# Optimization experiments

Hardware: AMD Instinct MI355X
Metric: run time of the kernel (lower is better)

## Reference

```python
import jax, jax.numpy as jnp
import numpy as np

WS = 14          # window size (SAM ViT default)
NUM_HEADS = 12   # dim=768 -> head_dim=64
THETA = 10000.0  # rope theta


def _axial_rope_cos_sin(head_dim, end_x, end_y):
    # compute_axial_cis: head_dim//4 freqs per axis; t_x = t % end_x, t_y = t // end_x
    n = head_dim // 4
    freqs = 1.0 / (THETA ** (np.arange(0, head_dim, 4)[:n].astype(np.float32) / head_dim))
    t = np.arange(end_x * end_y, dtype=np.float32)
    t_x = t % end_x
    t_y = np.floor(t / end_x)
    ang = np.concatenate([t_x[:, None] * freqs[None, :], t_y[:, None] * freqs[None, :]], axis=-1)
    return jnp.asarray(np.cos(ang)), jnp.asarray(np.sin(ang))  # (N, head_dim//2) each


def _apply_rope(x, cos, sin):
    # x: (B, N, D) viewed as complex pairs along last dim (torch.view_as_complex ordering)
    x2 = x.reshape(x.shape[:-1] + (-1, 2))
    xr, xi = x2[..., 0], x2[..., 1]
    out_r = xr * cos - xi * sin
    out_i = xr * sin + xi * cos
    return jnp.stack([out_r, out_i], axis=-1).reshape(x.shape)


def setup_inputs() -> dict:
    key = jax.random.key(0)
    ks = jax.random.split(key, 6)
    B, H, W, C = 8, 64, 64, 768
    hd = C // NUM_HEADS
    max_rel = 2 * WS - 1
    return {
        "x": jax.random.normal(ks[0], (B, H, W, C), dtype=jnp.float32),
        "qkv_w": jax.random.normal(ks[1], (3 * C, C), dtype=jnp.float32) * 0.02,
        "qkv_b": jnp.zeros((3 * C,), dtype=jnp.float32),
        "proj_w": jax.random.normal(ks[2], (C, C), dtype=jnp.float32) * 0.02,
        "proj_b": jnp.zeros((C,), dtype=jnp.float32),
        "rel_pos_h": jax.random.normal(ks[3], (max_rel, hd), dtype=jnp.float32) * 0.02,
        "rel_pos_w": jax.random.normal(ks[4], (max_rel, hd), dtype=jnp.float32) * 0.02,
    }


def reference(x, qkv_w, qkv_b, proj_w, proj_b, rel_pos_h, rel_pos_w):
    B, H, W, C = x.shape
    nH = NUM_HEADS
    hd = C // nH
    N = WS * WS

    # --- window_partition with padding ---
    pad_h = (-H) % WS
    pad_w = (-W) % WS
    xp = jnp.pad(x, ((0, 0), (0, pad_h), (0, pad_w), (0, 0)))
    Hp, Wp = H + pad_h, W + pad_w
    nwh, nww = Hp // WS, Wp // WS
    xw = xp.reshape(B, nwh, WS, nww, WS, C).transpose(0, 1, 3, 2, 4, 5).reshape(-1, N, C)
    Bw = xw.shape[0]  # B * num_windows

    # --- qkv projection, split heads ---
    qkv = xw @ qkv_w.T + qkv_b                       # (Bw, N, 3C)
    qkv = qkv.reshape(Bw, N, 3, nH, hd).transpose(2, 0, 3, 1, 4).reshape(3, Bw * nH, N, hd)
    q, k, v = qkv[0], qkv[1], qkv[2]

    # --- 2D axial rotary encoding on q, k ---
    cos, sin = _axial_rope_cos_sin(hd, WS, WS)       # (N, hd//2)
    q = _apply_rope(q, cos, sin)
    k = _apply_rope(k, cos, sin)

    # --- decomposed relative-position bias (get_rel_pos gather + einsum) ---
    coords = jnp.arange(WS)[:, None] - jnp.arange(WS)[None, :] + (WS - 1)  # (WS, WS) in [0, 2WS-2]
    Rh = rel_pos_h[coords]                           # (WS, WS, hd)
    Rw = rel_pos_w[coords]
    r_q = q.reshape(-1, WS, WS, hd)
    rel_h = jnp.einsum('bhwc,hkc->bhwk', r_q, Rh)    # (BwnH, WS, WS, WS)
    rel_w = jnp.einsum('bhwc,wkc->bhwk', r_q, Rw)

    # --- attention: q k^T / sqrt(hd) + rel biases (math of concat_rel_pos + sdpa) ---
    attn = jnp.einsum('bqc,bkc->bqk', q, k) * (hd ** -0.5)
    attn = attn.reshape(-1, WS, WS, WS, WS) + rel_h[..., :, None] + rel_w[..., None, :]
    attn = jax.nn.softmax(attn.reshape(-1, N, N), axis=-1)
    out = attn @ v                                   # (BwnH, N, hd)

    # --- merge heads, output projection ---
    out = out.reshape(Bw, nH, WS, WS, hd).transpose(0, 2, 3, 1, 4).reshape(Bw, N, C)
    out = out @ proj_w.T + proj_b

    # --- window_unpartition, crop padding ---
    out = out.reshape(B, nwh, nww, WS, WS, C).transpose(0, 1, 3, 2, 4, 5).reshape(B, Hp, Wp, C)
    return out[:, :H, :W, :]
```

## Files before the change

### kernel.cpp

```cpp
#include <hip/hip_runtime.h>

using u16 = unsigned short;
using u32 = unsigned int;

typedef __bf16 bf16x8 __attribute__((ext_vector_type(8)));
typedef float f32x4 __attribute__((ext_vector_type(4)));

#define M32 32768

__device__ __forceinline__ u16 f2bf(float f) {
  u32 u = __float_as_uint(f);
  u += 0x7fffu + ((u >> 16) & 1u);
  return (u16)(u >> 16);
}
__device__ __forceinline__ u32 cvtpk(float a, float b) {
  u32 r; asm("v_cvt_pk_bf16_f32 %0, %1, %2" : "=v"(r) : "v"(a), "v"(b)); return r;
}
__device__ __forceinline__ float bflo(u32 w) { return __uint_as_float(w << 16); }
__device__ __forceinline__ float bfhi(u32 w) { return __uint_as_float(w & 0xffff0000u); }

__device__ __forceinline__ float exp2h(float x) {
#if __has_builtin(__builtin_amdgcn_exp2f)
  return __builtin_amdgcn_exp2f(x);
#else
  float e; asm("v_exp_f32 %0, %1\n\ts_nop 0" : "=v"(e) : "v"(x)); return e;
#endif
}

__device__ __forceinline__ void async16(const void* g, void* l) {
  __builtin_amdgcn_global_load_lds((const __attribute__((address_space(1))) void*)g,
                                   (__attribute__((address_space(3))) void*)l, 16, 0, 0);
}

union frag { uint4 u; bf16x8 b; };

__global__ __launch_bounds__(256) void prep(const float* __restrict__ x, u16* __restrict__ xb,
                                            const float* __restrict__ qw, const float* __restrict__ pw,
                                            u16* __restrict__ qwb, u16* __restrict__ pwb,
                                            float2* __restrict__ cs) {
  int bid = blockIdx.x;
  if (bid < 12288) {
    size_t i = ((size_t)bid * 256 + threadIdx.x) * 8;
    float4 a = *(const float4*)(x + i);
    float4 b = *(const float4*)(x + i + 4);
    *(uint4*)(xb + i) = make_uint4(cvtpk(a.x, a.y), cvtpk(a.z, a.w),
                                   cvtpk(b.x, b.y), cvtpk(b.z, b.w));
  } else {
    int i = (bid - 12288) * 256 + threadIdx.x;
    if (i < 2304 * 768) qwb[i] = f2bf(qw[i]);
    if (i < 768 * 768)  pwb[i] = f2bf(pw[i]);
    if (i < 196 * 32) {
      int t = i >> 5, f = i & 31;
      float fr = powf(10000.f, -(float)(f & 15) * (1.f / 16.f));
      float ang = (f < 16 ? (float)(t % 14) : (float)(t / 14)) * fr;
      cs[i] = make_float2(cosf(ang), sinf(ang));
    }
  }
}

template<int EPI>
__global__ __launch_bounds__(256) void gemm_bt(
    const u16* __restrict__ A, const u16* __restrict__ B,
    const float* __restrict__ bias, u16* __restrict__ Cb,
    float* __restrict__ Cf, int K, int N, int NTI)
{
  __shared__ u16 As[3][128 * 32];
  __shared__ u16 Bs[3][128 * 32];

  const int nwg = gridDim.x;
  const int orig = blockIdx.x;
  const int q = nwg >> 3, r = nwg & 7;
  const int xcd = orig & 7, loc = orig >> 3;
  const int wg = (xcd < r ? xcd * (q + 1) : r * (q + 1) + (xcd - r) * q) + loc;
  const int m0 = (wg / NTI) * 128;
  const int n0 = (wg % NTI) * 128;

  const int tid = threadIdx.x;
  const int lane = tid & 63;
  const int wv = tid >> 6;
  const int wm = wv >> 1, wn = wv & 1;
  const int lr = lane & 15, lq = lane >> 4;

  const int srow0 = ((tid >> 6) << 4) + ((tid >> 2) & 15);
  const int sgsw  = ((tid & 3) ^ (((tid >> 5) & 1) << 1)) * 8;
  const u16* A0 = A + (size_t)(m0 + srow0) * K + sgsw;
  const u16* B0 = B + (size_t)(n0 + srow0) * K + sgsw;

  const int fro = lr * 32 + ((lq ^ (((lr >> 3) & 1) << 1)) << 3);

#define STAGE(buf, kk) { \
    async16(A0 + (kk), (void*)(As[buf] + tid * 8)); \
    async16(A0 + (size_t)64 * K + (kk), (void*)(As[buf] + 2048 + tid * 8)); \
    async16(B0 + (kk), (void*)(Bs[buf] + tid * 8)); \
    async16(B0 + (size_t)64 * K + (kk), (void*)(Bs[buf] + 2048 + tid * 8)); }

  STAGE(0, 0);
  STAGE(1, 32);
  asm volatile("s_waitcnt vmcnt(8)" ::: "memory");
  __builtin_amdgcn_s_barrier();

  f32x4 acc[4][4];
#pragma unroll
  for (int i = 0; i < 4; i++)
#pragma unroll
    for (int j = 0; j < 4; j++)
      acc[i][j] = f32x4{0.f, 0.f, 0.f, 0.f};

  const int NT = K / 32;
  for (int t = 0; t < NT; ++t) {
    const int cur = t % 3;
    const int nxt = (t + 2) % 3;
    const bool pre = (t + 2) < NT;

    if (pre) STAGE(nxt, (t + 2) * 32);

    const u16* Asc = As[cur];
    const u16* Bsc = Bs[cur];
    frag af[4], bg[4];
#pragma unroll
    for (int i = 0; i < 4; i++) {
      af[i].u = *(const uint4*)(Asc + (wm * 4 + i) * 512 + fro);
      bg[i].u = *(const uint4*)(Bsc + (wn * 4 + i) * 512 + fro);
    }

#pragma unroll
    for (int i = 0; i < 4; i++)
#pragma unroll
      for (int j = 0; j < 4; j++)
        acc[i][j] = __builtin_amdgcn_mfma_f32_16x16x32_bf16(af[i].b, bg[j].b, acc[i][j], 0, 0, 0);

    if (pre) { asm volatile("s_waitcnt vmcnt(8)" ::: "memory"); }
    else     { asm volatile("s_waitcnt vmcnt(0)" ::: "memory"); }
    __builtin_amdgcn_s_barrier();
  }
#undef STAGE

#pragma unroll
  for (int i = 0; i < 4; i++) {
#pragma unroll
    for (int j = 0; j < 4; j++) {
      const int n = n0 + wn * 64 + j * 16 + lr;
      const int mb = m0 + wm * 64 + i * 16 + lq * 4;
      const float bv = bias[n];
#pragma unroll
      for (int rr = 0; rr < 4; rr++) {
        float val = acc[i][j][rr] + bv;
        int m = mb + rr;
        if (EPI == 0) Cb[(size_t)m * N + n] = f2bf(val);
        else          Cf[(size_t)m * N + n] = val;
      }
    }
  }
}

#define R1P 104
#define VTP 232
#define PQP 40
#define LDS_R1   (224 * R1P * 2)
#define LDS_VT   (64 * VTP * 2)
#define LDS_PB   (4 * 16 * PQP * 2)
#define LDS_TOT  (LDS_R1 + LDS_VT + LDS_PB)

__global__ __launch_bounds__(256, 2) void attn_mfma(
    const u16* __restrict__ qkv, u16* __restrict__ ao,
    const float* __restrict__ relph, const float* __restrict__ relpw,
    const float2* __restrict__ cs, const float* __restrict__ qb)
{
  extern __shared__ char smem[];
  u16*   R1  = (u16*)smem;
  u16*   VTb = (u16*)(smem + LDS_R1);
  u16*   Th  = VTb;
  u16*   Tw  = VTb + 256 * 28;
  char*  PBr = smem + LDS_R1 + LDS_VT;

  const int orig = blockIdx.x;
  const int blk = (orig & 7) * 300 + (orig >> 3);
  const int w = blk / 12, h = blk % 12;
  const int tid = threadIdx.x;
  const int lane = tid & 63, wv = tid >> 6;
  const int lr = lane & 15, lq = lane >> 4;

  const int b0 = w / 25, rw_ = w % 25;
  const int wy = (rw_ / 5) * 14, wx = (rw_ % 5) * 14;
  const int ty = tid / 14, tx = tid - ty * 14;
  const int gh = wy + ty, gw = wx + tx;
  const bool inb = (tid < 196) && (gh < 64) && (gw < 64);
  const size_t grow = (size_t)((b0 * 64 + gh) * 64 + gw);

  {
    float qf[64];
    if (tid < 196) {
      if (inb) {
        const u16* qp = qkv + grow * 2304 + h * 64;
        uint4 q4[8];
#pragma unroll
        for (int u = 0; u < 8; u++) q4[u] = *(const uint4*)(qp + u * 8);
#pragma unroll
        for (int u = 0; u < 8; u++) {
          qf[u*8+0] = bflo(q4[u].x); qf[u*8+1] = bfhi(q4[u].x);
          qf[u*8+2] = bflo(q4[u].y); qf[u*8+3] = bfhi(q4[u].y);
          qf[u*8+4] = bflo(q4[u].z); qf[u*8+5] = bfhi(q4[u].z);
          qf[u*8+6] = bflo(q4[u].w); qf[u*8+7] = bfhi(q4[u].w);
        }
      } else {
        const float4* bp = (const float4*)(qb + h * 64);
#pragma unroll
        for (int u = 0; u < 16; u++) {
          float4 t4 = bp[u];
          qf[u*4+0] = t4.x; qf[u*4+1] = t4.y; qf[u*4+2] = t4.z; qf[u*4+3] = t4.w;
        }
      }
      const float2* ct = cs + tid * 32;
#pragma unroll
      for (int f = 0; f < 32; f++) {
        float2 c2 = ct[f];
        float xr = qf[2*f], xi = qf[2*f+1];
        qf[2*f]   = (xr * c2.x - xi * c2.y) * 0.18033688f;
        qf[2*f+1] = (xr * c2.y + xi * c2.x) * 0.18033688f;
      }
    } else {
#pragma unroll
      for (int d = 0; d < 64; d++) qf[d] = 0.f;
    }
    if (tid < 224) {
      u16* dst = R1 + tid * R1P;
#pragma unroll
      for (int u = 0; u < 8; u++)
        *(uint4*)(dst + u * 8) = make_uint4(cvtpk(qf[u*8+0], qf[u*8+1]), cvtpk(qf[u*8+2], qf[u*8+3]),
                                            cvtpk(qf[u*8+4], qf[u*8+5]), cvtpk(qf[u*8+6], qf[u*8+7]));
    }
  }

  uint4 k4[8], v4[8];
  if (inb) {
    const u16* kp = qkv + grow * 2304 + 768 + h * 64;
    const u16* vp = qkv + grow * 2304 + 1536 + h * 64;
#pragma unroll
    for (int u = 0; u < 8; u++) k4[u] = *(const uint4*)(kp + u * 8);
#pragma unroll
    for (int u = 0; u < 8; u++) v4[u] = *(const uint4*)(vp + u * 8);
  }
  __syncthreads();

  frag af[4][3];
#pragma unroll
  for (int i = 0; i < 4; i++)
#pragma unroll
    for (int kc = 0; kc < 2; kc++) {
      if (wv == 3 && i >= 2)
        af[i][kc].u = make_uint4(0u, 0u, 0u, 0u);
      else
        af[i][kc].u = *(const uint4*)(R1 + (wv * 64 + i * 16 + lr) * R1P + kc * 32 + lq * 8);
    }

#pragma unroll
  for (int n = 0; n < 2; n++) {
    f32x4 tah[4], taw[4];
#pragma unroll
    for (int i = 0; i < 4; i++) { tah[i] = f32x4{0,0,0,0}; taw[i] = f32x4{0,0,0,0}; }
    const int j = n * 16 + lr;
#pragma unroll
    for (int kc = 0; kc < 2; kc++) {
      float4 ha = {0,0,0,0}, hb = {0,0,0,0}, wa = {0,0,0,0}, wb2 = {0,0,0,0};
      if (j < 27) {
        const float* ph  = relph + j * 64 + kc * 32 + lq * 8;
        const float* pw2 = relpw + j * 64 + kc * 32 + lq * 8;
        ha = *(const float4*)ph;  hb  = *(const float4*)(ph + 4);
        wa = *(const float4*)pw2; wb2 = *(const float4*)(pw2 + 4);
      }
      frag bh, bw;
      bh.u = make_uint4(cvtpk(ha.x, ha.y), cvtpk(ha.z, ha.w), cvtpk(hb.x, hb.y), cvtpk(hb.z, hb.w));
      bw.u = make_uint4(cvtpk(wa.x, wa.y), cvtpk(wa.z, wa.w), cvtpk(wb2.x, wb2.y), cvtpk(wb2.z, wb2.w));
#pragma unroll
      for (int i = 0; i < 4; i++) {
        tah[i] = __builtin_amdgcn_mfma_f32_16x16x32_bf16(af[i][kc].b, bh.b, tah[i], 0, 0, 0);
        taw[i] = __builtin_amdgcn_mfma_f32_16x16x32_bf16(af[i][kc].b, bw.b, taw[i], 0, 0, 0);
      }
    }
    int jcol = n * 16 + lr;
    if (jcol < 28) {
#pragma unroll
      for (int i = 0; i < 4; i++)
#pragma unroll
        for (int r2 = 0; r2 < 4; r2++) {
          int qq = wv * 64 + i * 16 + lq * 4 + r2;
          Th[qq * 28 + jcol] = f2bf(tah[i][r2] * 8.f);
          Tw[qq * 28 + jcol] = f2bf(taw[i][r2] * 8.f);
        }
    }
  }
  __syncthreads();

  {
    u32 wb[16];
#pragma unroll
    for (int z = 0; z < 16; z++) wb[z] = 0;
    if (tid < 196) {
      const u16* thr = Th + tid * 28 + ty + 13;
      const u16* twr = Tw + tid * 28 + tx + 13;
#pragma unroll
      for (int p = 0; p < 7; p++) wb[p]     = (u32)thr[-(2*p)] | ((u32)thr[-(2*p+1)] << 16);
#pragma unroll
      for (int p = 0; p < 7; p++) wb[7 + p] = (u32)twr[-(2*p)] | ((u32)twr[-(2*p+1)] << 16);
    }
    wb[14] = 0xC22Du;
    if (tid < 224) {
      u16* dst = R1 + tid * R1P + 64;
#pragma unroll
      for (int u = 0; u < 4; u++)
        *(uint4*)(dst + u * 8) = make_uint4(wb[u*4], wb[u*4+1], wb[u*4+2], wb[u*4+3]);
    }
  }
  __syncthreads();

#pragma unroll
  for (int i = 0; i < 4; i++) {
    if (wv == 3 && i >= 2)
      af[i][2].u = make_uint4(0u, 0u, 0u, 0u);
    else
      af[i][2].u = *(const uint4*)(R1 + (wv * 64 + i * 16 + lr) * R1P + 64 + lq * 8);
  }
  __syncthreads();

  if (tid < 224) {
    const bool real = tid < 196;
    u32 kw[32];
#pragma unroll
    for (int z = 0; z < 32; z++) kw[z] = 0;
    if (real) {
      float kf[64];
      if (inb) {
#pragma unroll
        for (int u = 0; u < 8; u++) {
          kf[u*8+0] = bflo(k4[u].x); kf[u*8+1] = bfhi(k4[u].x);
          kf[u*8+2] = bflo(k4[u].y); kf[u*8+3] = bfhi(k4[u].y);
          kf[u*8+4] = bflo(k4[u].z); kf[u*8+5] = bfhi(k4[u].z);
          kf[u*8+6] = bflo(k4[u].w); kf[u*8+7] = bfhi(k4[u].w);
        }
      } else {
        const float4* bp = (const float4*)(qb + 768 + h * 64);
#pragma unroll
        for (int u = 0; u < 16; u++) {
          float4 t4 = bp[u];
          kf[u*4+0] = t4.x; kf[u*4+1] = t4.y; kf[u*4+2] = t4.z; kf[u*4+3] = t4.w;
        }
      }
      const float2* ct = cs + tid * 32;
#pragma unroll
      for (int f = 0; f < 32; f++) {
        float2 c2 = ct[f];
        float xr = kf[2*f], xi = kf[2*f+1];
        kf[2*f]   = xr * c2.x - xi * c2.y;
        kf[2*f+1] = xr * c2.y + xi * c2.x;
      }
#pragma unroll
      for (int p = 0; p < 32; p++) kw[p] = cvtpk(kf[2*p], kf[2*p+1]);
    }
    const int tA = real ? 64 + ty : 92;
    const int tB = real ? 78 + tx : 92;
    u32 aw[16];
#pragma unroll
    for (int p = 0; p < 16; p++) {
      const int c0 = 64 + 2 * p, c1 = c0 + 1;
      u32 lo = (c0 == tA || c0 == tB) ? 0x3F80u : 0u;
      u32 hi = (c1 == tA || c1 == tB) ? 0x3F80u : 0u;
      aw[p] = lo | (hi << 16);
    }
    u16* dst = R1 + tid * R1P;
#pragma unroll
    for (int u = 0; u < 8; u++)
      *(uint4*)(dst + u * 8) = make_uint4(kw[u*4], kw[u*4+1], kw[u*4+2], kw[u*4+3]);
#pragma unroll
    for (int u = 0; u < 4; u++)
      *(uint4*)(dst + 64 + u * 8) = make_uint4(aw[u*4], aw[u*4+1], aw[u*4+2], aw[u*4+3]);

    if (real) {
      u16* col = VTb + tid;
      if (inb) {
#pragma unroll
        for (int u = 0; u < 8; u++) {
          col[(u*8+0) * VTP] = (u16)(v4[u].x & 0xffff); col[(u*8+1) * VTP] = (u16)(v4[u].x >> 16);
          col[(u*8+2) * VTP] = (u16)(v4[u].y & 0xffff); col[(u*8+3) * VTP] = (u16)(v4[u].y >> 16);
          col[(u*8+4) * VTP] = (u16)(v4[u].z & 0xffff); col[(u*8+5) * VTP] = (u16)(v4[u].z >> 16);
          col[(u*8+6) * VTP] = (u16)(v4[u].w & 0xffff); col[(u*8+7) * VTP] = (u16)(v4[u].w >> 16);
        }
      } else {
        const float4* bp = (const float4*)(qb + 1536 + h * 64);
#pragma unroll
        for (int u = 0; u < 16; u++) {
          float4 t4 = bp[u];
          col[(u*4+0) * VTP] = f2bf(t4.x); col[(u*4+1) * VTP] = f2bf(t4.y);
          col[(u*4+2) * VTP] = f2bf(t4.z); col[(u*4+3) * VTP] = f2bf(t4.w);
        }
      }
    } else {
#pragma unroll
      for (int d = 0; d < 64; d++) VTb[d * VTP + tid] = 0;
    }
  }
  __syncthreads();

  f32x4 oacc[4][4];
  f32x4 lacc[4];
#pragma unroll
  for (int i = 0; i < 4; i++) {
    lacc[i] = f32x4{0,0,0,0};
#pragma unroll
    for (int j = 0; j < 4; j++) oacc[i][j] = f32x4{0,0,0,0};
  }
  frag ones;
  ones.u = make_uint4(0x3F803F80u, 0x3F803F80u, 0x3F803F80u, 0x3F803F80u);
  u16* PB = (u16*)PBr + wv * 16 * PQP;

  for (int c = 0; c < 7; c++) {
    frag bk[2][3];
#pragma unroll
    for (int kt = 0; kt < 2; kt++)
#pragma unroll
      for (int kc = 0; kc < 3; kc++)
        bk[kt][kc].u = *(const uint4*)(R1 + (c * 32 + kt * 16 + lr) * R1P + kc * 32 + lq * 8);

    frag bv[4];
#pragma unroll
    for (int j = 0; j < 4; j++)
      bv[j].u = *(const uint4*)(VTb + (j * 16 + lr) * VTP + c * 32 + lq * 8);

    f32x4 sacc[4][2];
#pragma unroll
    for (int i = 0; i < 4; i++) { sacc[i][0] = f32x4{0,0,0,0}; sacc[i][1] = f32x4{0,0,0,0}; }
#pragma unroll
    for (int kc = 0; kc < 3; kc++)
#pragma unroll
      for (int i = 0; i < 4; i++)
#pragma unroll
        for (int kt = 0; kt < 2; kt++)
          sacc[i][kt] = __builtin_amdgcn_mfma_f32_16x16x32_bf16(af[i][kc].b, bk[kt][kc].b, sacc[i][kt], 0, 0, 0);

#pragma unroll
    for (int i = 0; i < 4; i++) {
#pragma unroll
      for (int kt = 0; kt < 2; kt++)
#pragma unroll
        for (int r2 = 0; r2 < 4; r2++)
          PB[(lq * 4 + r2) * PQP + kt * 16 + lr] = f2bf(exp2h(sacc[i][kt][r2]));

      frag pf;
      pf.u = *(const uint4*)(PB + lr * PQP + lq * 8);

      lacc[i] = __builtin_amdgcn_mfma_f32_16x16x32_bf16(pf.b, ones.b, lacc[i], 0, 0, 0);
#pragma unroll
      for (int j = 0; j < 4; j++)
        oacc[i][j] = __builtin_amdgcn_mfma_f32_16x16x32_bf16(pf.b, bv[j].b, oacc[i][j], 0, 0, 0);
    }
  }

#pragma unroll
  for (int i = 0; i < 4; i++) {
    f32x4 inv;
#pragma unroll
    for (int r2 = 0; r2 < 4; r2++) inv[r2] = 1.f / lacc[i][r2];
#pragma unroll
    for (int r2 = 0; r2 < 4; r2++) {
      int qq = wv * 64 + i * 16 + lq * 4 + r2;
      if (qq < 196) {
        int qy = qq / 14, qx = qq - qy * 14;
        int gh2 = wy + qy, gw2 = wx + qx;
        if (gh2 < 64 && gw2 < 64) {
          u16* op = ao + (size_t)((b0 * 64 + gh2) * 64 + gw2) * 768 + h * 64 + lr;
#pragma unroll
          for (int j = 0; j < 4; j++)
            op[j * 16] = f2bf(oacc[i][j][r2] * inv[r2]);
        }
      }
    }
  }
}

extern "C" void kernel_launch(void* const* d_in, const int* in_sizes, int n_in,
                              void* d_out, int out_size, void* d_ws, size_t ws_size,
                              hipStream_t stream) {
  const float* x      = (const float*)d_in[0];
  const float* qkv_w  = (const float*)d_in[1];
  const float* qkv_b  = (const float*)d_in[2];
  const float* proj_w = (const float*)d_in[3];
  const float* proj_b = (const float*)d_in[4];
  const float* rel_h  = (const float*)d_in[5];
  const float* rel_w  = (const float*)d_in[6];
  float* out = (float*)d_out;

  char* ws = (char*)d_ws;
  u16* qkvb = (u16*)ws;
  u16* ao   = (u16*)(ws + (size_t)M32 * 2304 * 2);
  u16* qwb  = (u16*)(ws + (size_t)M32 * 2304 * 2 + (size_t)M32 * 768 * 2);
  u16* pwb  = qwb + 2304 * 768;
  float2* cs = (float2*)(pwb + 768 * 768);

  u16* xb = ao;

  prep<<<19200, 256, 0, stream>>>(x, xb, qkv_w, proj_w, qwb, pwb, cs);
  gemm_bt<0><<<dim3(256 * 18), 256, 0, stream>>>(xb, qwb, qkv_b, qkvb, nullptr, 768, 2304, 18);
  attn_mfma<<<2400, 256, LDS_TOT, stream>>>(qkvb, ao, rel_h, rel_w, cs, qkv_b);
  gemm_bt<1><<<dim3(256 * 6), 256, 0, stream>>>(ao, pwb, proj_b, nullptr, out, 768, 768, 6);
}
```

Baseline: 499.0 us.

## Load GEMM B fragments directly from global into registers, double-buffer A in LDS

The GEMM kernel no longer stages the B (weight) tile through shared memory. Each wave loads its B MFMA fragments directly from global memory into registers, while A stays staged through LDS with double buffering instead of triple buffering. This halves LDS use and removes the B LDS round trip. In exchange it adds per-wave redundant global loads of B, which now rely on cache hits, and a shallower prefetch depth guarded by full __syncthreads barriers.

```diff
diff --git a/kernel.cpp b/kernel.cpp
--- a/kernel.cpp
+++ b/kernel.cpp
@@ -64,8 +64,7 @@
     const float* __restrict__ bias, u16* __restrict__ Cb,
     float* __restrict__ Cf, int K, int N, int NTI)
 {
-  __shared__ u16 As[3][128 * 32];
-  __shared__ u16 Bs[3][128 * 32];
+  __shared__ u16 As[2][128 * 32];
 
   const int nwg = gridDim.x;
   const int orig = blockIdx.x;
@@ -84,20 +83,34 @@
   const int srow0 = ((tid >> 6) << 4) + ((tid >> 2) & 15);
   const int sgsw  = ((tid & 3) ^ (((tid >> 5) & 1) << 1)) * 8;
   const u16* A0 = A + (size_t)(m0 + srow0) * K + sgsw;
-  const u16* B0 = B + (size_t)(n0 + srow0) * K + sgsw;
 
   const int fro = lr * 32 + ((lq ^ (((lr >> 3) & 1) << 1)) << 3);
 
-#define STAGE(buf, kk) { \
+  const u16* Bq0 = B + (size_t)(n0 + wn * 64 + lr) * K + lq * 8;
+  const u16* Bq1 = Bq0 + (size_t)16 * K;
+  const u16* Bq2 = Bq0 + (size_t)32 * K;
+  const u16* Bq3 = Bq0 + (size_t)48 * K;
+
+#define STAGE_A(buf, kk) { \
     async16(A0 + (kk), (void*)(As[buf] + tid * 8)); \
-    async16(A0 + (size_t)64 * K + (kk), (void*)(As[buf] + 2048 + tid * 8)); \
-    async16(B0 + (kk), (void*)(Bs[buf] + tid * 8)); \
-    async16(B0 + (size_t)64 * K + (kk), (void*)(Bs[buf] + 2048 + tid * 8)); }
-
-  STAGE(0, 0);
-  STAGE(1, 32);
-  asm volatile("s_waitcnt vmcnt(8)" ::: "memory");
-  __builtin_amdgcn_s_barrier();
+    async16(A0 + (size_t)64 * K + (kk), (void*)(As[buf] + 2048 + tid * 8)); }
+
+#define LOADB(S, kk) { \
+    S[0].u = *(const uint4*)(Bq0 + (kk)); S[1].u = *(const uint4*)(Bq1 + (kk)); \
+    S[2].u = *(const uint4*)(Bq2 + (kk)); S[3].u = *(const uint4*)(Bq3 + (kk)); }
+
+#define MFMA16(af, bg) { \
+    _Pragma("unroll") \
+    for (int i = 0; i < 4; i++) \
+      _Pragma("unroll") \
+      for (int j = 0; j < 4; j++) \
+        acc[i][j] = __builtin_amdgcn_mfma_f32_16x16x32_bf16(af[i].b, bg[j].b, acc[i][j], 0, 0, 0); }
+
+  frag bA[4], bB[4];
+
+  STAGE_A(0, 0);
+  LOADB(bA, 0);
+  __syncthreads();
 
   f32x4 acc[4][4];
 #pragma unroll
@@ -107,33 +120,31 @@
       acc[i][j] = f32x4{0.f, 0.f, 0.f, 0.f};
 
   const int NT = K / 32;
-  for (int t = 0; t < NT; ++t) {
-    const int cur = t % 3;
-    const int nxt = (t + 2) % 3;
-    const bool pre = (t + 2) < NT;
-
-    if (pre) STAGE(nxt, (t + 2) * 32);
-
-    const u16* Asc = As[cur];
-    const u16* Bsc = Bs[cur];
-    frag af[4], bg[4];
-#pragma unroll
-    for (int i = 0; i < 4; i++) {
-      af[i].u = *(const uint4*)(Asc + (wm * 4 + i) * 512 + fro);
-      bg[i].u = *(const uint4*)(Bsc + (wn * 4 + i) * 512 + fro);
-    }
-
-#pragma unroll
-    for (int i = 0; i < 4; i++)
-#pragma unroll
-      for (int j = 0; j < 4; j++)
-        acc[i][j] = __builtin_amdgcn_mfma_f32_16x16x32_bf16(af[i].b, bg[j].b, acc[i][j], 0, 0, 0);
-
-    if (pre) { asm volatile("s_waitcnt vmcnt(8)" ::: "memory"); }
-    else     { asm volatile("s_waitcnt vmcnt(0)" ::: "memory"); }
-    __builtin_amdgcn_s_barrier();
-  }
-#undef STAGE
+  for (int t = 0; t < NT; t += 2) {
+    {
+      STAGE_A(1, (t + 1) * 32);
+      LOADB(bB, (t + 1) * 32);
+      frag af[4];
+#pragma unroll
+      for (int i = 0; i < 4; i++)
+        af[i].u = *(const uint4*)(As[0] + (wm * 4 + i) * 512 + fro);
+      MFMA16(af, bA);
+      __syncthreads();
+    }
+    {
+      const bool pre = (t + 2) < NT;
+      if (pre) { STAGE_A(0, (t + 2) * 32); LOADB(bA, (t + 2) * 32); }
+      frag af[4];
+#pragma unroll
+      for (int i = 0; i < 4; i++)
+        af[i].u = *(const uint4*)(As[1] + (wm * 4 + i) * 512 + fro);
+      MFMA16(af, bB);
+      __syncthreads();
+    }
+  }
+#undef STAGE_A
+#undef LOADB
+#undef MFMA16
 
 #pragma unroll
   for (int i = 0; i < 4; i++) {
```

Result: slower. 691.7 us (+38.6%).
